# Optimization experiments

Measured on AMD Instinct MI355X. Metric: run time of the kernel, lower is better.

Reference implementation:

```python
import jax, jax.numpy as jnp
import numpy as np
import math

B, L, D = 4, 4096, 1024
D_EMB, D_HID = 3, 16


def make_pos_emb(emb_dim, seq_len):
    # Complex exponential positional embeddings (non-trainable), shape (1, seq_len, emb_dim)
    t = np.linspace(0.0, 1.0, seq_len, dtype=np.float32)[None, :, None]
    bands = (emb_dim - 1) // 2
    t_res = np.linspace(0.0, seq_len - 1, seq_len, dtype=np.float32)[None, :, None]
    w = 2.0 * math.pi * t_res / seq_len
    f = np.linspace(0.0001, max(bands - 1, 0), bands, dtype=np.float32)[None, None]
    z = np.exp(-1j * (f * w).astype(np.complex64))
    z = np.concatenate([t, z.real.astype(np.float32), z.imag.astype(np.float32)], axis=-1)
    return jnp.asarray(z)


def setup_inputs() -> dict:
    key = jax.random.key(0)
    ks = jax.random.split(key, 8)
    u = jax.random.normal(ks[0], (B, L, D), dtype=jnp.float32)
    z = make_pos_emb(D_EMB, L)  # (1, L, D_EMB)
    # filter MLP: Linear(d_emb, d_hidden) -> ReLU -> Linear(d_hidden, d_model)
    s1 = 1.0 / math.sqrt(D_EMB)
    w1 = jax.random.uniform(ks[1], (D_HID, D_EMB), jnp.float32, -s1, s1)
    b1 = jax.random.uniform(ks[2], (D_HID,), jnp.float32, -s1, s1)
    s2 = 1.0 / math.sqrt(D_HID)
    w2 = jax.random.uniform(ks[3], (D, D_HID), jnp.float32, -s2, s2)
    b2 = jax.random.uniform(ks[4], (D,), jnp.float32, -s2, s2)
    # projection: Linear(d_model, d_model)
    sp = 1.0 / math.sqrt(D)
    pw = jax.random.uniform(ks[5], (D, D), jnp.float32, -sp, sp)
    pb = jax.random.uniform(ks[6], (D,), jnp.float32, -sp, sp)
    return {"u": u, "z": z, "w1": w1, "b1": b1, "w2": w2, "b2": b2, "pw": pw, "pb": pb}


def fft_conv(u_bdl, k_dl):
    # u_bdl: (B, D, L), k_dl: (1, D, L) or (D, L)
    seqlen = u_bdl.shape[-1]
    fft_size = 2 * seqlen
    k_f = jnp.fft.rfft(k_dl, n=fft_size) / fft_size
    u_f = jnp.fft.rfft(u_bdl, n=fft_size)
    y = jnp.fft.irfft(u_f * k_f, n=fft_size, norm="forward")[..., :seqlen]
    return y


def reference(u, z, w1, b1, w2, b2, pw, pb):
    seqlen = u.shape[1]
    pe = z[:, :seqlen]  # (1, L, D_EMB)
    h = jax.nn.relu(jnp.einsum("ble,he->blh", pe, w1) + b1)
    filt = jnp.einsum("blh,dh->bld", h, w2) + b2  # (1, L, D)
    filt = jnp.transpose(filt, (0, 2, 1))  # (1, D, L)
    u_conv = fft_conv(jnp.transpose(u, (0, 2, 1)), filt)  # (B, D, L)
    u_conv = jnp.transpose(u_conv, (0, 2, 1)).astype(u.dtype)  # (B, L, D)
    u_proj = jnp.einsum("bld,od->blo", u, pw) + pb
    return u_conv * u_proj + u
```

## Files before the change

### kernel.cpp

```cpp
#include <hip/hip_runtime.h>
#include <hip/hip_bf16.h>

#define SEQL 4096
#define DCH  1024
#define BATCH 4
#define KH   4097

typedef __attribute__((ext_vector_type(2))) float cf;
__device__ __forceinline__ cf mkc(float x, float y){ cf r; r.x = x; r.y = y; return r; }
__device__ __forceinline__ cf cadd(cf a, cf b){ return a + b; }
__device__ __forceinline__ cf csub(cf a, cf b){ return a - b; }
__device__ __forceinline__ cf cmul(cf a, cf b){ return a.xx * b + mkc(-a.y, a.y) * b.yx; }
__device__ __forceinline__ cf cconjf(cf a){ return mkc(a.x, -a.y); }
__device__ __forceinline__ cf addi(cf a, cf b){ return a + mkc(-b.y, b.x); }
__device__ __forceinline__ cf subi(cf a, cf b){ return a - mkc(-b.y, b.x); }
__device__ __forceinline__ int cpad(int i){ return i + (i >> 4); }
__device__ __forceinline__ int drev(int i){
    return ((i>>10)&3) | (((i>>8)&3)<<2) | (((i>>6)&3)<<4)
         | (((i>>4)&3)<<6) | (((i>>2)&3)<<8) | ((i&3)<<10);
}

__device__ __forceinline__ cf W1c(int j){
    const float cs[4] = {1.f, 0.92387953f, 0.70710678f, 0.38268343f};
    const float sn[4] = {0.f, -0.38268343f, -0.70710678f, -0.92387953f};
    return mkc(cs[j], sn[j]);
}
__device__ __forceinline__ cf W2c(int j){
    const float cs[4] = {1.f, 0.70710678f, 0.f, -0.70710678f};
    const float sn[4] = {0.f, -0.70710678f, -1.f, -0.70710678f};
    return mkc(cs[j], sn[j]);
}
__device__ __forceinline__ cf W3c(int j){
    const float cs[4] = {1.f, 0.38268343f, -0.70710678f, -0.92387953f};
    const float sn[4] = {0.f, -0.92387953f, -0.70710678f, 0.38268343f};
    return mkc(cs[j], sn[j]);
}

__device__ __forceinline__ unsigned pack2bf(float a, float b){
    unsigned r;
    asm("v_cvt_pk_bf16_f32 %0, %1, %2" : "=v"(r) : "v"(a), "v"(b));
    return r;
}
__device__ __forceinline__ float bflo(unsigned u){ return __uint_as_float(u << 16); }
__device__ __forceinline__ float bfhi(unsigned u){ return __uint_as_float(u & 0xffff0000u); }

__device__ __forceinline__ void gload16(const void* g, void* l){
    __builtin_amdgcn_global_load_lds((const __attribute__((address_space(1))) void*)g,
                                     (__attribute__((address_space(3))) void*)l, 16, 0, 0);
}

__global__ __launch_bounds__(256) void twiddle_init(cf* __restrict__ tw4, cf* __restrict__ tw8){
    int i = blockIdx.x*256 + threadIdx.x;
    const double TWO_PI = 6.283185307179586476925286766559;
    double a4 = -TWO_PI * (double)i / 4096.0;
    double a8 = -TWO_PI * (double)i / 8192.0;
    tw4[i] = mkc((float)cos(a4), (float)sin(a4));
    tw8[i] = mkc((float)cos(a8), (float)sin(a8));
}

__global__ __launch_bounds__(256) void mlp_kernel(
        const float* __restrict__ z, const float* __restrict__ w1,
        const float* __restrict__ b1, float* __restrict__ h) {
    int l = blockIdx.x * blockDim.x + threadIdx.x;
    if (l >= SEQL) return;
    float pe0 = z[l * 3 + 0], pe1 = z[l * 3 + 1], pe2 = z[l * 3 + 2];
#pragma unroll
    for (int j = 0; j < 16; ++j) {
        float v = pe0 * w1[j * 3 + 0] + pe1 * w1[j * 3 + 1] + pe2 * w1[j * 3 + 2] + b1[j];
        h[l * 16 + j] = v > 0.f ? v : 0.f;
    }
}

__global__ __launch_bounds__(256) void transpose_kernel(
        const float* __restrict__ u, float* __restrict__ ut,
        unsigned short* __restrict__ ub) {
    __shared__ float tile[32][33];
    int b = blockIdx.z;
    int l0 = blockIdx.x * 32;
    int d0 = blockIdx.y * 32;
    int tx = threadIdx.x, ty = threadIdx.y;
    const float* up = u + (size_t)b * SEQL * DCH;
    unsigned short* ubp = ub ? ub + (size_t)b * SEQL * DCH : (unsigned short*)0;
#pragma unroll
    for (int i = 0; i < 32; i += 8) {
        size_t idx = (size_t)(l0 + ty + i) * DCH + d0 + tx;
        float v = up[idx];
        tile[ty + i][tx] = v;
        if (ub) ubp[idx] = (unsigned short)pack2bf(v, v);
    }
    __syncthreads();
    float* utp = ut + (size_t)b * DCH * SEQL;
#pragma unroll
    for (int i = 0; i < 32; i += 8)
        utp[(size_t)(d0 + ty + i) * SEQL + l0 + tx] = tile[tx][ty + i];
}

__global__ __launch_bounds__(256) void pw2bf_kernel(
        const float* __restrict__ pw, unsigned short* __restrict__ pwb) {
    int t = blockIdx.x * 256 + threadIdx.x;
    float4 a = *(const float4*)&pw[(size_t)t * 8];
    float4 b = *(const float4*)&pw[(size_t)t * 8 + 4];
    uint4 o;
    o.x = pack2bf(a.x, a.y); o.y = pack2bf(a.z, a.w);
    o.z = pack2bf(b.x, b.y); o.w = pack2bf(b.z, b.w);
    *(uint4*)&pwb[(size_t)t * 8] = o;
}

__device__ void dif_mid_and_chunk(cf* lds, const cf* __restrict__ tw){
    const int tid = threadIdx.x;
#pragma unroll
    for (int p = 1; p < 4; ++p) {
        const int lm = 10 - 2*p;
        const int m  = 1 << lm;
        const int step = 1024 >> lm;
#pragma unroll
        for (int it = 0; it < 4; ++it) {
            int j = tid + (it << 8);
            int k = j & (m-1);
            int g = j >> lm;
            int i0 = (g << (lm+2)) + k;
            cf x0 = lds[cpad(i0)];
            cf x1 = lds[cpad(i0+m)];
            cf x2 = lds[cpad(i0+2*m)];
            cf x3 = lds[cpad(i0+3*m)];
            cf b0 = cadd(x0,x2), b1 = csub(x0,x2);
            cf b2 = cadd(x1,x3), b3 = csub(x1,x3);
            cf u0 = cadd(b0,b2);
            cf u2 = csub(b0,b2);
            cf u1 = subi(b1,b3);
            cf u3 = addi(b1,b3);
            int t1 = k*step;
            lds[cpad(i0)]     = u0;
            lds[cpad(i0+m)]   = cmul(u1, tw[t1]);
            lds[cpad(i0+2*m)] = cmul(u2, tw[2*t1]);
            lds[cpad(i0+3*m)] = cmul(u3, tw[3*t1]);
        }
        __syncthreads();
    }
    {
        int base = 17*tid;
        cf v[16];
#pragma unroll
        for (int j=0;j<16;++j) v[j] = lds[base+j];
#pragma unroll
        for (int j=0;j<4;++j){
            cf x0=v[j], x1=v[j+4], x2=v[j+8], x3=v[j+12];
            cf b0=cadd(x0,x2), b1=csub(x0,x2), b2=cadd(x1,x3), b3=csub(x1,x3);
            cf u0=cadd(b0,b2), u2=csub(b0,b2), u1=subi(b1,b3), u3=addi(b1,b3);
            v[j]    = u0;
            v[j+4]  = cmul(u1, W1c(j));
            v[j+8]  = cmul(u2, W2c(j));
            v[j+12] = cmul(u3, W3c(j));
        }
#pragma unroll
        for (int c=0;c<4;++c){
            cf x0=v[4*c], x1=v[4*c+1], x2=v[4*c+2], x3=v[4*c+3];
            cf b0=cadd(x0,x2), b1=csub(x0,x2), b2=cadd(x1,x3), b3=csub(x1,x3);
            v[4*c]   = cadd(b0,b2);
            v[4*c+1] = subi(b1,b3);
            v[4*c+2] = csub(b0,b2);
            v[4*c+3] = addi(b1,b3);
        }
#pragma unroll
        for (int j=0;j<16;++j) lds[base+j] = v[j];
        __syncthreads();
    }
}

__device__ void dit_chunk_and_mid(cf* lds, const cf* __restrict__ tw){
    const int tid = threadIdx.x;
    {
        int base = 17*tid;
        cf v[16];
#pragma unroll
        for (int j=0;j<16;++j) v[j] = lds[base+j];
#pragma unroll
        for (int c=0;c<4;++c){
            cf a0=v[4*c], a1=v[4*c+1], a2=v[4*c+2], a3=v[4*c+3];
            cf b0=cadd(a0,a2), b1=csub(a0,a2), b2=cadd(a1,a3), b3=csub(a1,a3);
            v[4*c]   = cadd(b0,b2);
            v[4*c+1] = addi(b1,b3);
            v[4*c+2] = csub(b0,b2);
            v[4*c+3] = subi(b1,b3);
        }
#pragma unroll
        for (int j=0;j<4;++j){
            cf a0=v[j];
            cf a1=cmul(v[j+4],  cconjf(W1c(j)));
            cf a2=cmul(v[j+8],  cconjf(W2c(j)));
            cf a3=cmul(v[j+12], cconjf(W3c(j)));
            cf b0=cadd(a0,a2), b1=csub(a0,a2), b2=cadd(a1,a3), b3=csub(a1,a3);
            v[j]    = cadd(b0,b2);
            v[j+4]  = addi(b1,b3);
            v[j+8]  = csub(b0,b2);
            v[j+12] = subi(b1,b3);
        }
#pragma unroll
        for (int j=0;j<16;++j) lds[base+j] = v[j];
        __syncthreads();
    }
#pragma unroll
    for (int p = 0; p < 3; ++p) {
        const int lm = 4 + 2*p;
        const int m  = 1 << lm;
        const int step = 1024 >> lm;
#pragma unroll
        for (int it = 0; it < 4; ++it) {
            int j = tid + (it << 8);
            int k = j & (m-1);
            int g = j >> lm;
            int i0 = (g << (lm+2)) + k;
            int t1 = k*step;
            cf a0 = lds[cpad(i0)];
            cf a1 = cmul(lds[cpad(i0+m)],   cconjf(tw[t1]));
            cf a2 = cmul(lds[cpad(i0+2*m)], cconjf(tw[2*t1]));
            cf a3 = cmul(lds[cpad(i0+3*m)], cconjf(tw[3*t1]));
            cf b0=cadd(a0,a2), b1=csub(a0,a2), b2=cadd(a1,a3), b3=csub(a1,a3);
            lds[cpad(i0)]     = cadd(b0,b2);
            lds[cpad(i0+m)]   = addi(b1,b3);
            lds[cpad(i0+2*m)] = csub(b0,b2);
            lds[cpad(i0+3*m)] = subi(b1,b3);
        }
        __syncthreads();
    }
}

__global__ __launch_bounds__(256) void filt_fft_kernel(
        const float* __restrict__ h, const float* __restrict__ w2,
        const float* __restrict__ b2, const cf* __restrict__ tw4,
        const cf* __restrict__ tw8, cf* __restrict__ kf) {
    __shared__ cf lds[4352];
    const int d = blockIdx.x;
    const int tid = threadIdx.x;
    float wv[16];
#pragma unroll
    for (int j = 0; j < 16; ++j) wv[j] = w2[d * 16 + j];
    const float bb = b2[d];
#pragma unroll
    for (int it = 0; it < 4; ++it) {
        int j = tid + (it << 8);
        const float* h0 = h + (size_t)(2*j) * 16;
        const float* h1 = h + (size_t)(2*(j+1024)) * 16;
        float f0 = bb, f1 = bb, f2 = bb, f3 = bb;
#pragma unroll
        for (int i = 0; i < 16; ++i) {
            f0 += h0[i] * wv[i];  f1 += h0[16+i] * wv[i];
            f2 += h1[i] * wv[i];  f3 += h1[16+i] * wv[i];
        }
        cf x0 = mkc(f0, f1), x1 = mkc(f2, f3);
        cf u0 = cadd(x0,x1);
        cf u2 = csub(x0,x1);
        cf u1 = subi(x0,x1);
        cf u3 = addi(x0,x1);
        lds[cpad(j)]      = u0;
        lds[cpad(j+1024)] = cmul(u1, tw4[j]);
        lds[cpad(j+2048)] = cmul(u2, tw4[2*j]);
        lds[cpad(j+3072)] = cmul(u3, tw4[3*j]);
    }
    __syncthreads();
    dif_mid_and_chunk(lds, tw4);
    const float s = 1.f / 8192.f;
    cf* Hrow = kf + (size_t)d * KH;
    const int lane  = tid & 63;
    const int kbase = ((lane & 31) << 6) | ((lane >> 5) << 5) | ((tid >> 6) << 3);
#pragma unroll
    for (int it = 0; it < 8; ++it) {
        int k = kbase + it;
        if (k == 0) {
            cf c0 = lds[cpad(0)];
            Hrow[0]    = mkc((c0.x + c0.y) * s, 0.f);
            Hrow[4096] = mkc((c0.x - c0.y) * s, 0.f);
            cf c2 = lds[cpad(drev(2048))];
            Hrow[2048] = mkc(c2.x * s, -c2.y * s);
        } else {
            int kk = 4096 - k;
            cf ck  = lds[cpad(drev(k))];
            cf ckk = lds[cpad(drev(kk))];
            cf cc = cconjf(ckk);
            cf E  = (ck + cc) * 0.5f;
            cf Dd = csub(ck, cc);
            cf O  = mkc(Dd.y, -Dd.x) * 0.5f;
            cf wvv = tw8[k];
            cf Xk  = cadd(E, cmul(wvv, O));
            cf wp  = mkc(-wvv.x, wvv.y);
            cf Xkk = cadd(cconjf(E), cmul(wp, cconjf(O)));
            Hrow[k]  = Xk * s;
            Hrow[kk] = Xkk * s;
        }
    }
}

__global__ __launch_bounds__(256) void conv_kernel(
        float* __restrict__ uty, const cf* __restrict__ tw4,
        const cf* __restrict__ tw8, const cf* __restrict__ kf) {
    __shared__ cf lds[4352];
    const int row = blockIdx.x;
    const int d = row & (DCH - 1);
    const int tid = threadIdx.x;
    float* rp = uty + (size_t)row * SEQL;
#pragma unroll
    for (int it = 0; it < 4; ++it) {
        int j = tid + (it << 8);
        cf x0 = *(const cf*)&rp[2*j];
        cf x1 = *(const cf*)&rp[2*(j+1024)];
        cf u0 = cadd(x0,x1);
        cf u2 = csub(x0,x1);
        cf u1 = subi(x0,x1);
        cf u3 = addi(x0,x1);
        lds[cpad(j)]      = u0;
        lds[cpad(j+1024)] = cmul(u1, tw4[j]);
        lds[cpad(j+2048)] = cmul(u2, tw4[2*j]);
        lds[cpad(j+3072)] = cmul(u3, tw4[3*j]);
    }
    __syncthreads();
    dif_mid_and_chunk(lds, tw4);
    const cf* Hrow = kf + (size_t)d * KH;
    {
        const int lane  = tid & 63;
        const int kbase = ((lane & 31) << 6) | ((lane >> 5) << 5) | ((tid >> 6) << 3);
#pragma unroll
        for (int it = 0; it < 8; ++it) {
            int k = kbase + it;
            if (k == 0) {
                cf c0 = lds[cpad(0)];
                float X0 = c0.x + c0.y, X4 = c0.x - c0.y;
                cf H0 = Hrow[0], H4 = Hrow[4096];
                cf Y0 = H0 * X0;
                cf Y4 = H4 * X4;
                cf S  = cadd(Y0, Y4), Dd = csub(Y0, Y4);
                lds[cpad(0)] = addi(S, Dd);
                int s2 = cpad(drev(2048));
                cf c2 = lds[s2];
                cf Y2 = cmul(cconjf(c2), Hrow[2048]);
                lds[s2] = mkc(2.f * Y2.x, -2.f * Y2.y);
            } else {
                int kk = 4096 - k;
                int sk = cpad(drev(k)), skk = cpad(drev(kk));
                cf ck = lds[sk], ckk = lds[skk];
                cf cc = cconjf(ckk);
                cf E  = (ck + cc) * 0.5f;
                cf Dd = csub(ck, cc);
                cf O  = mkc(Dd.y, -Dd.x) * 0.5f;
                cf wv = tw8[k];
                cf Xk  = cadd(E, cmul(wv, O));
                cf wp  = mkc(-wv.x, wv.y);
                cf Xkk = cadd(cconjf(E), cmul(wp, cconjf(O)));
                cf Yk  = cmul(Xk,  Hrow[k]);
                cf Ykk = cmul(Xkk, Hrow[kk]);
                cf cy = cconjf(Ykk);
                cf S  = cadd(Yk, cy), D2 = csub(Yk, cy);
                cf Zk = addi(S, cmul(cconjf(wv), D2));
                cf cy2 = cconjf(Yk);
                cf S2  = cadd(Ykk, cy2), D3 = csub(Ykk, cy2);
                cf Zkk = subi(S2, cmul(wv, D3));
                lds[sk] = Zk; lds[skk] = Zkk;
            }
        }
    }
    __syncthreads();
    dit_chunk_and_mid(lds, tw4);
    unsigned short* yb = (unsigned short*)rp;
#pragma unroll
    for (int it = 0; it < 4; ++it) {
        int j = tid + (it << 8);
        cf a0 = lds[cpad(j)];
        cf a1 = cmul(lds[cpad(j+1024)], cconjf(tw4[j]));
        cf a2 = cmul(lds[cpad(j+2048)], cconjf(tw4[2*j]));
        cf a3 = cmul(lds[cpad(j+3072)], cconjf(tw4[3*j]));
        cf b0 = cadd(a0,a2), b1 = csub(a0,a2);
        cf b2 = cadd(a1,a3), b3 = csub(a1,a3);
        cf o0 = cadd(b0,b2);
        cf o1 = addi(b1,b3);
        *(unsigned*)&yb[2*j]          = pack2bf(o0.x, o0.y);
        *(unsigned*)&yb[2*(j+1024)]   = pack2bf(o1.x, o1.y);
    }
}

typedef __attribute__((ext_vector_type(8))) short short8;
typedef __attribute__((ext_vector_type(4))) float f32x4;

__global__ __launch_bounds__(256, 4) void gemm_mfma_v2(
        const unsigned short* __restrict__ ub, const unsigned short* __restrict__ pwb,
        const float* __restrict__ pb, const unsigned short* __restrict__ yb,
        float* __restrict__ out) {
    __shared__ char lds_raw[34816];
    float (*ysc)[132] = (float(*)[132])lds_raw;

    const int tid  = threadIdx.x;
    const int lane = tid & 63;
    const int wid  = tid >> 6;
    const int wr   = wid >> 1;
    const int wc   = wid & 1;
    const int m0   = blockIdx.x * 128;
    const int n0   = blockIdx.y * 128;

    f32x4 acc[4][4] = {};

    const int srow = lane >> 2;
    const int scol = 16 * ((lane & 3) ^ ((lane >> 2) & 3));

#define STAGE2(bufbase, kt)                                                                   \
    {                                                                                         \
        _Pragma("unroll")                                                                     \
        for (int i = 0; i < 2; ++i) {                                                         \
            int c = wid * 2 + i;                                                              \
            const char* gA = (const char*)ub  + (size_t)(m0 + c * 16 + srow) * 2048 + (kt) * 2 + scol; \
            const char* gB = (const char*)pwb + (size_t)(n0 + c * 16 + srow) * 2048 + (kt) * 2 + scol; \
            gload16(gA, lds_raw + (bufbase) + c * 1024);                                      \
            gload16(gB, lds_raw + (bufbase) + 8192 + c * 1024);                               \
        }                                                                                     \
    }

    STAGE2(0, 0);
    __syncthreads();

    for (int t = 0; t < 32; ++t) {
        const int cur = (t & 1) << 14;
        if (t < 31) STAGE2(cur ^ 16384, (t + 1) * 32);
        short8 af[4], bfr[4];
#pragma unroll
        for (int f = 0; f < 4; ++f) {
            int rowA = wr * 64 + f * 16 + (lane & 15);
            int rowB = wc * 64 + f * 16 + (lane & 15);
            int offA = cur + rowA * 64 + (((lane >> 4) * 16) ^ ((rowA & 3) << 4));
            int offB = cur + 8192 + rowB * 64 + (((lane >> 4) * 16) ^ ((rowB & 3) << 4));
            af[f]  = *(short8*)(lds_raw + offA);
            bfr[f] = *(short8*)(lds_raw + offB);
        }
#pragma unroll
        for (int mf = 0; mf < 4; ++mf)
#pragma unroll
            for (int nf = 0; nf < 4; ++nf)
                acc[mf][nf] = __builtin_amdgcn_mfma_f32_16x16x32_bf16(
                    af[mf], bfr[nf], acc[mf][nf], 0, 0, 0);
        __syncthreads();
    }

    const int b  = m0 >> 12;
    const int l0 = m0 & (SEQL - 1);
    float pbv[4];
#pragma unroll
    for (int nf = 0; nf < 4; ++nf)
        pbv[nf] = pb[n0 + wc * 64 + nf * 16 + (lane & 15)];

    for (int c = 0; c < 2; ++c) {
        __syncthreads();
#pragma unroll
        for (int j = 0; j < 4; ++j) {
            int idx = j * 256 + tid;
            int dn  = idx >> 3;
            int lg  = idx & 7;
            uint4 w4 = *(const uint4*)&yb[(((size_t)(b * DCH + n0 + dn)) << 13) + l0 + c * 64 + lg * 8];
            int lb = lg * 8;
            ysc[lb+0][dn] = bflo(w4.x); ysc[lb+1][dn] = bfhi(w4.x);
            ysc[lb+2][dn] = bflo(w4.y); ysc[lb+3][dn] = bfhi(w4.y);
            ysc[lb+4][dn] = bflo(w4.z); ysc[lb+5][dn] = bfhi(w4.z);
            ysc[lb+6][dn] = bflo(w4.w); ysc[lb+7][dn] = bfhi(w4.w);
        }
        __syncthreads();
        if (wr == c) {
#pragma unroll
            for (int mf = 0; mf < 4; ++mf)
#pragma unroll
                for (int i = 0; i < 4; ++i) {
                    int lrow = mf * 16 + (lane >> 4) * 4 + i;
                    int m = m0 + c * 64 + lrow;
#pragma unroll
                    for (int nf = 0; nf < 4; ++nf) {
                        int nl = wc * 64 + nf * 16 + (lane & 15);
                        int n = n0 + nl;
                        float proj = acc[mf][nf][i] + pbv[nf];
                        float ures = __uint_as_float((unsigned)ub[(size_t)m * DCH + n] << 16);
                        out[(size_t)m * DCH + n] = ysc[lrow][nl] * proj + ures;
                    }
                }
        }
    }
#undef STAGE2
}

__global__ __launch_bounds__(256, 3) void gemm_mfma_fb(
        const float* __restrict__ u, const float* __restrict__ pw,
        const float* __restrict__ pb, const unsigned short* __restrict__ yb,
        float* __restrict__ out) {
    __shared__ char lds_raw[34816];
    float (*ysc)[132] = (float(*)[132])lds_raw;
    const int tid  = threadIdx.x;
    const int lane = tid & 63;
    const int wid  = tid >> 6;
    const int wr   = wid >> 1;
    const int wc   = wid & 1;
    const int m0   = blockIdx.x * 128;
    const int n0   = blockIdx.y * 128;
    f32x4 acc[4][4] = {};
    float4 ra[4], rb[4];
    int s_row[4], s_f4[4];
#pragma unroll
    for (int j = 0; j < 4; ++j) {
        int idx = j * 256 + tid;
        s_row[j] = idx >> 3;
        s_f4[j]  = idx & 7;
    }
#define LOADT(kt)                                                                     \
    {                                                                                 \
        _Pragma("unroll")                                                             \
        for (int j = 0; j < 4; ++j) {                                                 \
            ra[j] = *(const float4*)&u [(size_t)(m0 + s_row[j]) * DCH + (kt) + s_f4[j] * 4]; \
            rb[j] = *(const float4*)&pw[(size_t)(n0 + s_row[j]) * DCH + (kt) + s_f4[j] * 4]; \
        }                                                                             \
    }
#define WRITET(base)                                                                  \
    {                                                                                 \
        _Pragma("unroll")                                                             \
        for (int j = 0; j < 4; ++j) {                                                 \
            int off = (base) + ((s_row[j] * 64 + s_f4[j] * 8) ^ ((s_row[j] & 3) << 4)); \
            uint2 pa, pbv2;                                                           \
            pa.x   = pack2bf(ra[j].x, ra[j].y);  pa.y   = pack2bf(ra[j].z, ra[j].w);  \
            pbv2.x = pack2bf(rb[j].x, rb[j].y);  pbv2.y = pack2bf(rb[j].z, rb[j].w);  \
            *(uint2*)(lds_raw + off)        = pa;                                     \
            *(uint2*)(lds_raw + off + 8192) = pbv2;                                   \
        }                                                                             \
    }
    LOADT(0);
    WRITET(0);
    LOADT(32);
    __syncthreads();
    for (int t = 0; t < 32; ++t) {
        const int cur = (t & 1) << 14;
        short8 af[4], bfr[4];
#pragma unroll
        for (int f = 0; f < 4; ++f) {
            int rowA = wr * 64 + f * 16 + (lane & 15);
            int rowB = wc * 64 + f * 16 + (lane & 15);
            int offA = cur + ((rowA * 64 + ((lane >> 4) * 16)) ^ ((rowA & 3) << 4));
            int offB = cur + 8192 + ((rowB * 64 + ((lane >> 4) * 16)) ^ ((rowB & 3) << 4));
            af[f]  = *(short8*)(lds_raw + offA);
            bfr[f] = *(short8*)(lds_raw + offB);
        }
        if (t < 31) WRITET(cur ^ 16384);
        if (t < 30) LOADT((t + 2) * 32);
#pragma unroll
        for (int mf = 0; mf < 4; ++mf)
#pragma unroll
            for (int nf = 0; nf < 4; ++nf)
                acc[mf][nf] = __builtin_amdgcn_mfma_f32_16x16x32_bf16(
                    af[mf], bfr[nf], acc[mf][nf], 0, 0, 0);
        __syncthreads();
    }
    const int b  = m0 >> 12;
    const int l0 = m0 & (SEQL - 1);
    float pbv[4];
#pragma unroll
    for (int nf = 0; nf < 4; ++nf)
        pbv[nf] = pb[n0 + wc * 64 + nf * 16 + (lane & 15)];
    for (int c = 0; c < 2; ++c) {
        __syncthreads();
#pragma unroll
        for (int j = 0; j < 4; ++j) {
            int idx = j * 256 + tid;
            int dn  = idx >> 3;
            int lg  = idx & 7;
            uint4 w4 = *(const uint4*)&yb[(((size_t)(b * DCH + n0 + dn)) << 13) + l0 + c * 64 + lg * 8];
            int lb = lg * 8;
            ysc[lb+0][dn] = bflo(w4.x); ysc[lb+1][dn] = bfhi(w4.x);
            ysc[lb+2][dn] = bflo(w4.y); ysc[lb+3][dn] = bfhi(w4.y);
            ysc[lb+4][dn] = bflo(w4.z); ysc[lb+5][dn] = bfhi(w4.z);
            ysc[lb+6][dn] = bflo(w4.w); ysc[lb+7][dn] = bfhi(w4.w);
        }
        __syncthreads();
        if (wr == c) {
#pragma unroll
            for (int mf = 0; mf < 4; ++mf)
#pragma unroll
                for (int i = 0; i < 4; ++i) {
                    int lrow = mf * 16 + (lane >> 4) * 4 + i;
                    int m = m0 + c * 64 + lrow;
#pragma unroll
                    for (int nf = 0; nf < 4; ++nf) {
                        int nl = wc * 64 + nf * 16 + (lane & 15);
                        int n = n0 + nl;
                        float proj = acc[mf][nf][i] + pbv[nf];
                        out[(size_t)m * DCH + n] = ysc[lrow][nl] * proj + u[(size_t)m * DCH + n];
                    }
                }
        }
    }
#undef LOADT
#undef WRITET
}

extern "C" void kernel_launch(void* const* d_in, const int* in_sizes, int n_in,
                              void* d_out, int out_size, void* d_ws, size_t ws_size,
                              hipStream_t stream) {
    const float* u  = (const float*)d_in[0];
    const float* z  = (const float*)d_in[1];
    const float* w1 = (const float*)d_in[2];
    const float* b1 = (const float*)d_in[3];
    const float* w2 = (const float*)d_in[4];
    const float* b2 = (const float*)d_in[5];
    const float* pw = (const float*)d_in[6];
    const float* pb = (const float*)d_in[7];
    float* out = (float*)d_out;

    float* h   = (float*)d_ws;
    float* uty = (float*)((char*)d_ws + 262144);
    cf* kf = (cf*)d_out;

    const size_t ub_off  = 262144 + (size_t)BATCH * DCH * SEQL * sizeof(float);
    const size_t pwb_off = ub_off + (size_t)BATCH * SEQL * DCH * sizeof(unsigned short);
    const size_t tw_off  = pwb_off + (size_t)DCH * DCH * sizeof(unsigned short);
    const size_t need    = tw_off + 2 * 4096 * sizeof(cf);
    const bool   big     = ws_size >= need;

    cf* tw4 = big ? (cf*)((char*)d_ws + tw_off) : (cf*)((char*)d_out + (40u << 20));
    cf* tw8 = tw4 + 4096;
    unsigned short* ub  = big ? (unsigned short*)((char*)d_ws + ub_off)  : (unsigned short*)0;
    unsigned short* pwb = big ? (unsigned short*)((char*)d_ws + pwb_off) : (unsigned short*)0;

    twiddle_init<<<dim3(16), dim3(256), 0, stream>>>(tw4, tw8);
    mlp_kernel<<<dim3(16), dim3(256), 0, stream>>>(z, w1, b1, h);
    transpose_kernel<<<dim3(SEQL / 32, DCH / 32, BATCH), dim3(32, 8), 0, stream>>>(u, uty, ub);
    if (big) pw2bf_kernel<<<dim3(512), dim3(256), 0, stream>>>(pw, pwb);
    filt_fft_kernel<<<dim3(DCH), dim3(256), 0, stream>>>(h, w2, b2, tw4, tw8, kf);
    conv_kernel<<<dim3(BATCH * DCH), dim3(256), 0, stream>>>(uty, tw4, tw8, kf);
    if (big)
        gemm_mfma_v2<<<dim3(128, 8), dim3(256), 0, stream>>>(ub, pwb, pb, (const unsigned short*)uty, out);
    else
        gemm_mfma_fb<<<dim3(128, 8), dim3(256), 0, stream>>>(u, pw, pb, (const unsigned short*)uty, out);
}
```

Measured before the change: 273.7 us.

## Store transposed input as bf16, compact conv output rows, XOR-swizzle FFT LDS

The transpose kernel now writes the transposed input as packed bf16 pairs instead of fp32. The conv kernel reads those bf16 values and writes its bf16 output into the same compact row buffer, so the GEMM epilogue uses a halved row stride. The padded LDS layout for the FFTs is replaced by an XOR swizzle, which shrinks shared memory from 4352 to 4096 complex entries. This cuts global traffic for the transposed intermediate and LDS footprint, at the cost of rounding the conv input to bf16.

```diff
diff --git a/kernel.cpp b/kernel.cpp
--- a/kernel.cpp
+++ b/kernel.cpp
@@ -14,7 +14,7 @@
 __device__ __forceinline__ cf cconjf(cf a){ return mkc(a.x, -a.y); }
 __device__ __forceinline__ cf addi(cf a, cf b){ return a + mkc(-b.y, b.x); }
 __device__ __forceinline__ cf subi(cf a, cf b){ return a - mkc(-b.y, b.x); }
-__device__ __forceinline__ int cpad(int i){ return i + (i >> 4); }
+__device__ __forceinline__ int phi(int c){ return c ^ ((c >> 4) & 15); }
 __device__ __forceinline__ int drev(int i){
     return ((i>>10)&3) | (((i>>8)&3)<<2) | (((i>>6)&3)<<4)
          | (((i>>4)&3)<<6) | (((i>>2)&3)<<8) | ((i&3)<<10);
@@ -72,7 +72,7 @@
 }
 
 __global__ __launch_bounds__(256) void transpose_kernel(
-        const float* __restrict__ u, float* __restrict__ ut,
+        const float* __restrict__ u, unsigned* __restrict__ utb,
         unsigned short* __restrict__ ub) {
     __shared__ float tile[32][33];
     int b = blockIdx.z;
@@ -89,10 +89,16 @@
         if (ub) ubp[idx] = (unsigned short)pack2bf(v, v);
     }
     __syncthreads();
-    float* utp = ut + (size_t)b * DCH * SEQL;
-#pragma unroll
-    for (int i = 0; i < 32; i += 8)
-        utp[(size_t)(d0 + ty + i) * SEQL + l0 + tx] = tile[tx][ty + i];
+    unsigned* utp = utb + (size_t)b * DCH * (SEQL / 2);
+    int t  = ty * 32 + tx;
+    int dl = t >> 4;
+    int lp = t & 15;
+#pragma unroll
+    for (int p = 0; p < 2; ++p) {
+        int dd = dl + p * 16;
+        unsigned v = pack2bf(tile[2 * lp][dd], tile[2 * lp + 1][dd]);
+        utp[(size_t)(d0 + dd) * (SEQL / 2) + (l0 >> 1) + lp] = v;
+    }
 }
 
 __global__ __launch_bounds__(256) void pw2bf_kernel(
@@ -119,10 +125,10 @@
             int k = j & (m-1);
             int g = j >> lm;
             int i0 = (g << (lm+2)) + k;
-            cf x0 = lds[cpad(i0)];
-            cf x1 = lds[cpad(i0+m)];
-            cf x2 = lds[cpad(i0+2*m)];
-            cf x3 = lds[cpad(i0+3*m)];
+            cf x0 = lds[phi(i0)];
+            cf x1 = lds[phi(i0+m)];
+            cf x2 = lds[phi(i0+2*m)];
+            cf x3 = lds[phi(i0+3*m)];
             cf b0 = cadd(x0,x2), b1 = csub(x0,x2);
             cf b2 = cadd(x1,x3), b3 = csub(x1,x3);
             cf u0 = cadd(b0,b2);
@@ -130,23 +136,24 @@
             cf u1 = subi(b1,b3);
             cf u3 = addi(b1,b3);
             int t1 = k*step;
-            lds[cpad(i0)]     = u0;
-            lds[cpad(i0+m)]   = cmul(u1, tw[t1]);
-            lds[cpad(i0+2*m)] = cmul(u2, tw[2*t1]);
-            lds[cpad(i0+3*m)] = cmul(u3, tw[3*t1]);
+            lds[phi(i0)]     = u0;
+            lds[phi(i0+m)]   = cmul(u1, tw[t1]);
+            lds[phi(i0+2*m)] = cmul(u2, tw[2*t1]);
+            lds[phi(i0+3*m)] = cmul(u3, tw[3*t1]);
         }
         __syncthreads();
     }
     {
-        int base = 17*tid;
+        const int b0 = tid << 4;
+        const int xr = tid & 15;
         cf v[16];
 #pragma unroll
-        for (int j=0;j<16;++j) v[j] = lds[base+j];
+        for (int j=0;j<16;++j) v[j] = lds[b0 + (j ^ xr)];
 #pragma unroll
         for (int j=0;j<4;++j){
             cf x0=v[j], x1=v[j+4], x2=v[j+8], x3=v[j+12];
-            cf b0=cadd(x0,x2), b1=csub(x0,x2), b2=cadd(x1,x3), b3=csub(x1,x3);
-            cf u0=cadd(b0,b2), u2=csub(b0,b2), u1=subi(b1,b3), u3=addi(b1,b3);
+            cf b0v=cadd(x0,x2), b1=csub(x0,x2), b2=cadd(x1,x3), b3=csub(x1,x3);
+            cf u0=cadd(b0v,b2), u2=csub(b0v,b2), u1=subi(b1,b3), u3=addi(b1,b3);
             v[j]    = u0;
             v[j+4]  = cmul(u1, W1c(j));
             v[j+8]  = cmul(u2, W2c(j));
@@ -155,14 +162,14 @@
 #pragma unroll
         for (int c=0;c<4;++c){
             cf x0=v[4*c], x1=v[4*c+1], x2=v[4*c+2], x3=v[4*c+3];
-            cf b0=cadd(x0,x2), b1=csub(x0,x2), b2=cadd(x1,x3), b3=csub(x1,x3);
-            v[4*c]   = cadd(b0,b2);
+            cf b0v=cadd(x0,x2), b1=csub(x0,x2), b2=cadd(x1,x3), b3=csub(x1,x3);
+            v[4*c]   = cadd(b0v,b2);
             v[4*c+1] = subi(b1,b3);
-            v[4*c+2] = csub(b0,b2);
+            v[4*c+2] = csub(b0v,b2);
             v[4*c+3] = addi(b1,b3);
         }
 #pragma unroll
-        for (int j=0;j<16;++j) lds[base+j] = v[j];
+        for (int j=0;j<16;++j) lds[b0 + (j ^ xr)] = v[j];
         __syncthreads();
     }
 }
@@ -170,17 +177,18 @@
 __device__ void dit_chunk_and_mid(cf* lds, const cf* __restrict__ tw){
     const int tid = threadIdx.x;
     {
-        int base = 17*tid;
+        const int b0 = tid << 4;
+        const int xr = tid & 15;
         cf v[16];
 #pragma unroll
-        for (int j=0;j<16;++j) v[j] = lds[base+j];
+        for (int j=0;j<16;++j) v[j] = lds[b0 + (j ^ xr)];
 #pragma unroll
         for (int c=0;c<4;++c){
             cf a0=v[4*c], a1=v[4*c+1], a2=v[4*c+2], a3=v[4*c+3];
-            cf b0=cadd(a0,a2), b1=csub(a0,a2), b2=cadd(a1,a3), b3=csub(a1,a3);
-            v[4*c]   = cadd(b0,b2);
+            cf b0v=cadd(a0,a2), b1=csub(a0,a2), b2=cadd(a1,a3), b3=csub(a1,a3);
+            v[4*c]   = cadd(b0v,b2);
             v[4*c+1] = addi(b1,b3);
-            v[4*c+2] = csub(b0,b2);
+            v[4*c+2] = csub(b0v,b2);
             v[4*c+3] = subi(b1,b3);
         }
 #pragma unroll
@@ -189,14 +197,14 @@
             cf a1=cmul(v[j+4],  cconjf(W1c(j)));
             cf a2=cmul(v[j+8],  cconjf(W2c(j)));
             cf a3=cmul(v[j+12], cconjf(W3c(j)));
-            cf b0=cadd(a0,a2), b1=csub(a0,a2), b2=cadd(a1,a3), b3=csub(a1,a3);
-            v[j]    = cadd(b0,b2);
+            cf b0v=cadd(a0,a2), b1=csub(a0,a2), b2=cadd(a1,a3), b3=csub(a1,a3);
+            v[j]    = cadd(b0v,b2);
             v[j+4]  = addi(b1,b3);
-            v[j+8]  = csub(b0,b2);
+            v[j+8]  = csub(b0v,b2);
             v[j+12] = subi(b1,b3);
         }
 #pragma unroll
-        for (int j=0;j<16;++j) lds[base+j] = v[j];
+        for (int j=0;j<16;++j) lds[b0 + (j ^ xr)] = v[j];
         __syncthreads();
     }
 #pragma unroll
@@ -211,15 +219,15 @@
             int g = j >> lm;
             int i0 = (g << (lm+2)) + k;
             int t1 = k*step;
-            cf a0 = lds[cpad(i0)];
-            cf a1 = cmul(lds[cpad(i0+m)],   cconjf(tw[t1]));
-            cf a2 = cmul(lds[cpad(i0+2*m)], cconjf(tw[2*t1]));
-            cf a3 = cmul(lds[cpad(i0+3*m)], cconjf(tw[3*t1]));
+            cf a0 = lds[phi(i0)];
+            cf a1 = cmul(lds[phi(i0+m)],   cconjf(tw[t1]));
+            cf a2 = cmul(lds[phi(i0+2*m)], cconjf(tw[2*t1]));
+            cf a3 = cmul(lds[phi(i0+3*m)], cconjf(tw[3*t1]));
             cf b0=cadd(a0,a2), b1=csub(a0,a2), b2=cadd(a1,a3), b3=csub(a1,a3);
-            lds[cpad(i0)]     = cadd(b0,b2);
-            lds[cpad(i0+m)]   = addi(b1,b3);
-            lds[cpad(i0+2*m)] = csub(b0,b2);
-            lds[cpad(i0+3*m)] = subi(b1,b3);
+            lds[phi(i0)]     = cadd(b0,b2);
+            lds[phi(i0+m)]   = addi(b1,b3);
+            lds[phi(i0+2*m)] = csub(b0,b2);
+            lds[phi(i0+3*m)] = subi(b1,b3);
         }
         __syncthreads();
     }
@@ -229,7 +237,7 @@
         const float* __restrict__ h, const float* __restrict__ w2,
         const float* __restrict__ b2, const cf* __restrict__ tw4,
         const cf* __restrict__ tw8, cf* __restrict__ kf) {
-    __shared__ cf lds[4352];
+    __shared__ cf lds[4096];
     const int d = blockIdx.x;
     const int tid = threadIdx.x;
     float wv[16];
@@ -252,10 +260,10 @@
         cf u2 = csub(x0,x1);
         cf u1 = subi(x0,x1);
         cf u3 = addi(x0,x1);
-        lds[cpad(j)]      = u0;
-        lds[cpad(j+1024)] = cmul(u1, tw4[j]);
-        lds[cpad(j+2048)] = cmul(u2, tw4[2*j]);
-        lds[cpad(j+3072)] = cmul(u3, tw4[3*j]);
+        lds[phi(j)]      = u0;
+        lds[phi(j+1024)] = cmul(u1, tw4[j]);
+        lds[phi(j+2048)] = cmul(u2, tw4[2*j]);
+        lds[phi(j+3072)] = cmul(u3, tw4[3*j]);
     }
     __syncthreads();
     dif_mid_and_chunk(lds, tw4);
@@ -267,15 +275,15 @@
     for (int it = 0; it < 8; ++it) {
         int k = kbase + it;
         if (k == 0) {
-            cf c0 = lds[cpad(0)];
+            cf c0 = lds[0];
             Hrow[0]    = mkc((c0.x + c0.y) * s, 0.f);
             Hrow[4096] = mkc((c0.x - c0.y) * s, 0.f);
-            cf c2 = lds[cpad(drev(2048))];
+            cf c2 = lds[phi(drev(2048))];
             Hrow[2048] = mkc(c2.x * s, -c2.y * s);
         } else {
             int kk = 4096 - k;
-            cf ck  = lds[cpad(drev(k))];
-            cf ckk = lds[cpad(drev(kk))];
+            cf ck  = lds[phi(drev(k))];
+            cf ckk = lds[phi(drev(kk))];
             cf cc = cconjf(ckk);
             cf E  = (ck + cc) * 0.5f;
             cf Dd = csub(ck, cc);
@@ -291,26 +299,27 @@
 }
 
 __global__ __launch_bounds__(256) void conv_kernel(
-        float* __restrict__ uty, const cf* __restrict__ tw4,
+        unsigned* __restrict__ utyb, const cf* __restrict__ tw4,
         const cf* __restrict__ tw8, const cf* __restrict__ kf) {
-    __shared__ cf lds[4352];
+    __shared__ cf lds[4096];
     const int row = blockIdx.x;
     const int d = row & (DCH - 1);
     const int tid = threadIdx.x;
-    float* rp = uty + (size_t)row * SEQL;
+    unsigned* rp = utyb + (size_t)row * (SEQL / 2);
 #pragma unroll
     for (int it = 0; it < 4; ++it) {
         int j = tid + (it << 8);
-        cf x0 = *(const cf*)&rp[2*j];
-        cf x1 = *(const cf*)&rp[2*(j+1024)];
+        unsigned q0 = rp[j], q1 = rp[j + 1024];
+        cf x0 = mkc(bflo(q0), bfhi(q0));
+        cf x1 = mkc(bflo(q1), bfhi(q1));
         cf u0 = cadd(x0,x1);
         cf u2 = csub(x0,x1);
         cf u1 = subi(x0,x1);
         cf u3 = addi(x0,x1);
-        lds[cpad(j)]      = u0;
-        lds[cpad(j+1024)] = cmul(u1, tw4[j]);
-        lds[cpad(j+2048)] = cmul(u2, tw4[2*j]);
-        lds[cpad(j+3072)] = cmul(u3, tw4[3*j]);
+        lds[phi(j)]      = u0;
+        lds[phi(j+1024)] = cmul(u1, tw4[j]);
+        lds[phi(j+2048)] = cmul(u2, tw4[2*j]);
+        lds[phi(j+3072)] = cmul(u3, tw4[3*j]);
     }
     __syncthreads();
     dif_mid_and_chunk(lds, tw4);
@@ -322,20 +331,20 @@
         for (int it = 0; it < 8; ++it) {
             int k = kbase + it;
             if (k == 0) {
-                cf c0 = lds[cpad(0)];
+                cf c0 = lds[0];
                 float X0 = c0.x + c0.y, X4 = c0.x - c0.y;
                 cf H0 = Hrow[0], H4 = Hrow[4096];
                 cf Y0 = H0 * X0;
                 cf Y4 = H4 * X4;
                 cf S  = cadd(Y0, Y4), Dd = csub(Y0, Y4);
-                lds[cpad(0)] = addi(S, Dd);
-                int s2 = cpad(drev(2048));
+                lds[0] = addi(S, Dd);
+                int s2 = phi(drev(2048));
                 cf c2 = lds[s2];
                 cf Y2 = cmul(cconjf(c2), Hrow[2048]);
                 lds[s2] = mkc(2.f * Y2.x, -2.f * Y2.y);
             } else {
                 int kk = 4096 - k;
-                int sk = cpad(drev(k)), skk = cpad(drev(kk));
+                int sk = phi(drev(k)), skk = phi(drev(kk));
                 cf ck = lds[sk], ckk = lds[skk];
                 cf cc = cconjf(ckk);
                 cf E  = (ck + cc) * 0.5f;
@@ -359,20 +368,19 @@
     }
     __syncthreads();
     dit_chunk_and_mid(lds, tw4);
-    unsigned short* yb = (unsigned short*)rp;
 #pragma unroll
     for (int it = 0; it < 4; ++it) {
         int j = tid + (it << 8);
-        cf a0 = lds[cpad(j)];
-        cf a1 = cmul(lds[cpad(j+1024)], cconjf(tw4[j]));
-        cf a2 = cmul(lds[cpad(j+2048)], cconjf(tw4[2*j]));
-        cf a3 = cmul(lds[cpad(j+3072)], cconjf(tw4[3*j]));
+        cf a0 = lds[phi(j)];
+        cf a1 = cmul(lds[phi(j+1024)], cconjf(tw4[j]));
+        cf a2 = cmul(lds[phi(j+2048)], cconjf(tw4[2*j]));
+        cf a3 = cmul(lds[phi(j+3072)], cconjf(tw4[3*j]));
         cf b0 = cadd(a0,a2), b1 = csub(a0,a2);
         cf b2 = cadd(a1,a3), b3 = csub(a1,a3);
         cf o0 = cadd(b0,b2);
         cf o1 = addi(b1,b3);
-        *(unsigned*)&yb[2*j]          = pack2bf(o0.x, o0.y);
-        *(unsigned*)&yb[2*(j+1024)]   = pack2bf(o1.x, o1.y);
+        rp[j]        = pack2bf(o0.x, o0.y);
+        rp[j + 1024] = pack2bf(o1.x, o1.y);
     }
 }
 
@@ -450,7 +458,7 @@
             int idx = j * 256 + tid;
             int dn  = idx >> 3;
             int lg  = idx & 7;
-            uint4 w4 = *(const uint4*)&yb[(((size_t)(b * DCH + n0 + dn)) << 13) + l0 + c * 64 + lg * 8];
+            uint4 w4 = *(const uint4*)&yb[(((size_t)(b * DCH + n0 + dn)) << 12) + l0 + c * 64 + lg * 8];
             int lb = lg * 8;
             ysc[lb+0][dn] = bflo(w4.x); ysc[lb+1][dn] = bfhi(w4.x);
             ysc[lb+2][dn] = bflo(w4.y); ysc[lb+3][dn] = bfhi(w4.y);
@@ -560,7 +568,7 @@
             int idx = j * 256 + tid;
             int dn  = idx >> 3;
             int lg  = idx & 7;
-            uint4 w4 = *(const uint4*)&yb[(((size_t)(b * DCH + n0 + dn)) << 13) + l0 + c * 64 + lg * 8];
+            uint4 w4 = *(const uint4*)&yb[(((size_t)(b * DCH + n0 + dn)) << 12) + l0 + c * 64 + lg * 8];
             int lb = lg * 8;
             ysc[lb+0][dn] = bflo(w4.x); ysc[lb+1][dn] = bfhi(w4.x);
             ysc[lb+2][dn] = bflo(w4.y); ysc[lb+3][dn] = bfhi(w4.y);
@@ -602,11 +610,11 @@
     const float* pb = (const float*)d_in[7];
     float* out = (float*)d_out;
 
-    float* h   = (float*)d_ws;
-    float* uty = (float*)((char*)d_ws + 262144);
+    float*    h    = (float*)d_ws;
+    unsigned* utyb = (unsigned*)((char*)d_ws + 262144);
     cf* kf = (cf*)d_out;
 
-    const size_t ub_off  = 262144 + (size_t)BATCH * DCH * SEQL * sizeof(float);
+    const size_t ub_off  = 262144 + (size_t)BATCH * DCH * (SEQL / 2) * sizeof(unsigned);
     const size_t pwb_off = ub_off + (size_t)BATCH * SEQL * DCH * sizeof(unsigned short);
     const size_t tw_off  = pwb_off + (size_t)DCH * DCH * sizeof(unsigned short);
     const size_t need    = tw_off + 2 * 4096 * sizeof(cf);
@@ -619,12 +627,12 @@
 
     twiddle_init<<<dim3(16), dim3(256), 0, stream>>>(tw4, tw8);
     mlp_kernel<<<dim3(16), dim3(256), 0, stream>>>(z, w1, b1, h);
-    transpose_kernel<<<dim3(SEQL / 32, DCH / 32, BATCH), dim3(32, 8), 0, stream>>>(u, uty, ub);
+    transpose_kernel<<<dim3(SEQL / 32, DCH / 32, BATCH), dim3(32, 8), 0, stream>>>(u, utyb, ub);
     if (big) pw2bf_kernel<<<dim3(512), dim3(256), 0, stream>>>(pw, pwb);
     filt_fft_kernel<<<dim3(DCH), dim3(256), 0, stream>>>(h, w2, b2, tw4, tw8, kf);
-    conv_kernel<<<dim3(BATCH * DCH), dim3(256), 0, stream>>>(uty, tw4, tw8, kf);
+    conv_kernel<<<dim3(BATCH * DCH), dim3(256), 0, stream>>>(utyb, tw4, tw8, kf);
     if (big)
-        gemm_mfma_v2<<<dim3(128, 8), dim3(256), 0, stream>>>(ub, pwb, pb, (const unsigned short*)uty, out);
+        gemm_mfma_v2<<<dim3(128, 8), dim3(256), 0, stream>>>(ub, pwb, pb, (const unsigned short*)utyb, out);
     else
-        gemm_mfma_fb<<<dim3(128, 8), dim3(256), 0, stream>>>(u, pw, pb, (const unsigned short*)uty, out);
-}
+        gemm_mfma_fb<<<dim3(128, 8), dim3(256), 0, stream>>>(u, pw, pb, (const unsigned short*)utyb, out);
+}
```

After: 266.4 us. 2.7% less time.
